# Performance work log

Measured on AMD Instinct MI355X. Metric: run time of the kernel, lower is better.

## Reference

```python
import math
import jax, jax.numpy as jnp
import numpy as np

B, SX, SY, D, H = 2, 1024, 1024, 1024, 16
FULL = 1536   # padded (full_q == full_k) frame length for the two-source attention
N_CTX = 2048  # causal bias buffer size
HD = D // H
LENS_X = np.array([1024, 700])
LENS_Y = np.array([1024, 850])


def _heads(t):
    b, s, d = t.shape
    return t.reshape(b, s, H, HD).transpose(0, 2, 1, 3)  # [B,H,S,HD]


def _merge(t):
    b, h, s, hd = t.shape
    return t.transpose(0, 2, 1, 3).reshape(b, s, h * hd)


def setup_inputs() -> dict:
    key = jax.random.key(0)
    ks = jax.random.split(key, 8)
    s = 0.02
    # ragged pack/unpack index lists: take = positions in the FULL frame, fill = positions in the shrunk frame
    x_take_b = np.concatenate([np.full(l, b, np.int32) for b, l in enumerate(LENS_X)])
    x_take_p = np.concatenate([(FULL - l + np.arange(l)).astype(np.int32) for l in LENS_X])  # right-aligned
    x_fill_b = x_take_b.copy()
    x_fill_p = np.concatenate([np.arange(l, dtype=np.int32) for l in LENS_X])
    y_take_b = np.concatenate([np.full(l, b, np.int32) for b, l in enumerate(LENS_Y)])
    y_take_p = np.concatenate([np.arange(l, dtype=np.int32) for l in LENS_Y])  # left-aligned
    y_fill_b = y_take_b.copy()
    y_fill_p = y_take_p.copy()
    # additive padding mask for the self-attention over shrunk x
    mask = np.full((B, 1, 1, SX), -10000.0, np.float32)
    for b, l in enumerate(LENS_X):
        mask[b, :, :, :l] = 0.0
    return {
        "x": jax.random.normal(ks[0], (B, SX, D), jnp.float32),
        "y": jax.random.normal(ks[1], (B, SY, D), jnp.float32),
        "attention_mask_x": jnp.asarray(mask),
        "W_attn": jax.random.normal(ks[2], (D, 3 * D), jnp.float32) * s,
        "b_attn": jnp.zeros((3 * D,), jnp.float32),
        "W_2a": jax.random.normal(ks[3], (D, D), jnp.float32) * s,
        "b_2a": jnp.zeros((D,), jnp.float32),
        "W_2b": jax.random.normal(ks[4], (D, 2 * D), jnp.float32) * s,
        "b_2b": jnp.zeros((2 * D,), jnp.float32),
        "W_proj": jax.random.normal(ks[5], (2 * D, D), jnp.float32) * s,
        "b_proj": jnp.zeros((D,), jnp.float32),
        "x_take_b": jnp.asarray(x_take_b), "x_take_p": jnp.asarray(x_take_p),
        "x_fill_b": jnp.asarray(x_fill_b), "x_fill_p": jnp.asarray(x_fill_p),
        "y_take_b": jnp.asarray(y_take_b), "y_take_p": jnp.asarray(y_take_p),
        "y_fill_b": jnp.asarray(y_fill_b), "y_fill_p": jnp.asarray(y_fill_p),
    }


def reference(x, y, attention_mask_x, W_attn, b_attn, W_2a, b_2a, W_2b, b_2b,
              W_proj, b_proj, x_take_b, x_take_p, x_fill_b, x_fill_p,
              y_take_b, y_take_p, y_fill_b, y_fill_p):
    causal = jnp.tril(jnp.ones((N_CTX, N_CTX), jnp.float32))
    inv_sqrt = 1.0 / math.sqrt(HD)

    # --- branch 1: causal self-attention on shrunk x ---
    qkv = x @ W_attn + b_attn
    q, k, v = jnp.split(qkv, 3, axis=2)
    q, k, v = _heads(q), _heads(k), _heads(v)
    w = jnp.einsum('bhqd,bhkd->bhqk', q, k) * inv_sqrt  # [B,H,SX,SX]
    b1 = causal[:SX, :SX]
    w = w * b1 - 10000.0 * (1.0 - b1) + attention_mask_x
    a = jnp.einsum('bhqk,bhkd->bhqd', jax.nn.softmax(w, axis=-1), v)
    a = _merge(a)  # [B,SX,D]

    # --- branch 2: two-source attention with ragged expand/shrink ---
    q2 = _heads(x @ W_2a + b_2a)                      # [B,H,SX,HD]
    k2, v2 = jnp.split(y @ W_2b + b_2b, 2, axis=2)
    k2, v2 = _heads(k2), _heads(v2)                   # [B,H,SY,HD]
    w2 = jnp.einsum('bhqd,bhkd->bhqk', q2, k2)        # [B,H,SX,SY] (unscaled yet)
    # expand key dim: shrunk SY -> FULL
    temp = jnp.zeros((B, H, SX, FULL), w2.dtype)
    temp = temp.at[y_take_b, :, :, y_take_p].set(w2[y_fill_b, :, :, y_fill_p])
    # expand query dim: shrunk SX -> FULL
    new_w = jnp.zeros((B, H, FULL, FULL), w2.dtype)
    new_w = new_w.at[x_take_b, :, x_take_p, :].set(temp[x_fill_b, :, x_fill_p, :])
    new_v = jnp.zeros((B, H, FULL, HD), v2.dtype)
    new_v = new_v.at[y_take_b, :, y_take_p, :].set(v2[y_fill_b, :, y_fill_p, :])
    kmask = jnp.full((B, 1, 1, FULL), -10000.0, w2.dtype)
    kmask = kmask.at[y_take_b, :, :, y_take_p].set(0.0)
    new_w = new_w * inv_sqrt
    b2 = causal[:FULL, :FULL]  # ns-nd == 0 since full_q == full_k
    new_w = new_w * b2 - 10000.0 * (1.0 - b2) + kmask
    a2 = jnp.einsum('bhqk,bhkd->bhqd', jax.nn.softmax(new_w, axis=-1), new_v)  # [B,H,FULL,HD]
    # shrink query dim back: FULL -> SX
    a2s = jnp.zeros((B, H, SX, HD), a2.dtype)
    a2s = a2s.at[x_fill_b, :, x_fill_p, :].set(a2[x_take_b, :, x_take_p, :])
    a2m = _merge(a2s)  # [B,SX,D]

    out = jnp.concatenate([a, a2m], axis=2) @ W_proj + b_proj  # [B,SX,D]
    return out
```

## Files before the change

### kernel.cpp

```cpp
#include <hip/hip_runtime.h>
#include <hip/hip_bf16.h>

typedef __bf16 bf16;
typedef __attribute__((ext_vector_type(4))) __bf16 bf16x4;
typedef __attribute__((ext_vector_type(8))) __bf16 bf16x8;
typedef __attribute__((ext_vector_type(4))) float floatx4;

__device__ __forceinline__ void gl_lds16(const bf16* g, bf16* l) {
  __builtin_amdgcn_global_load_lds(
      (const __attribute__((address_space(1))) void*)g,
      (__attribute__((address_space(3))) void*)l, 16, 0, 0);
}

__global__ __launch_bounds__(256) void sentinel_kernel(float* out, int n, float code) {
  int i = blockIdx.x * 256 + threadIdx.x;
  if (i < n) out[i] = code;
}

struct TP { const float* W; bf16* WT; int K; int N; int bxn; int bid0; };

__global__ __launch_bounds__(256) void prep_kernel(TP t0, TP t1, TP t2, TP t3,
                                                   const float* __restrict__ x,
                                                   const float* __restrict__ y,
                                                   bf16* __restrict__ xb,
                                                   bf16* __restrict__ yb) {
  int bid = blockIdx.x;
  int tid = threadIdx.x;
  if (bid < 2048) {
    __shared__ float tile[64][65];
    TP t = t0;
    if (bid >= t3.bid0) t = t3;
    else if (bid >= t2.bid0) t = t2;
    else if (bid >= t1.bid0) t = t1;
    int rb = bid - t.bid0;
    int n0 = (rb % t.bxn) * 64, k0 = (rb / t.bxn) * 64;
    int tx = tid & 15, ty = tid >> 4;
#pragma unroll
    for (int i = 0; i < 4; ++i) {
      floatx4 v = *(const floatx4*)(t.W + (size_t)(k0 + ty + 16 * i) * t.N + n0 + tx * 4);
#pragma unroll
      for (int j = 0; j < 4; ++j) tile[ty + 16 * i][tx * 4 + j] = v[j];
    }
    __syncthreads();
#pragma unroll
    for (int i = 0; i < 4; ++i) {
      int nr = ty + 16 * i;
      bf16x4 o;
#pragma unroll
      for (int j = 0; j < 4; ++j) o[j] = (bf16)tile[tx * 4 + j][nr];
      *(bf16x4*)(t.WT + (size_t)(n0 + nr) * t.K + k0 + tx * 4) = o;
    }
  } else {
    long base = (long)(bid - 2048) * 4096 + (long)tid * 16;
    const float* src = x; bf16* dst = xb; long idx = base;
    if (base >= 2097152) { src = y; dst = yb; idx = base - 2097152; }
    floatx4 v0 = *(const floatx4*)(src + idx);
    floatx4 v1 = *(const floatx4*)(src + idx + 4);
    floatx4 v2 = *(const floatx4*)(src + idx + 8);
    floatx4 v3 = *(const floatx4*)(src + idx + 12);
    bf16x8 o0, o1;
#pragma unroll
    for (int i = 0; i < 4; ++i) {
      o0[i] = (bf16)v0[i]; o0[4 + i] = (bf16)v1[i];
      o1[i] = (bf16)v2[i]; o1[4 + i] = (bf16)v3[i];
    }
    *(bf16x8*)(dst + idx) = o0;
    *(bf16x8*)(dst + idx + 8) = o1;
  }
}

struct GP { const bf16* A; const bf16* WT; const float* bias; bf16* C; bf16* VT;
            int N; int ldc; int vcol0; int bxn; int bid0; };

__global__ __launch_bounds__(256) void proj3_kernel(GP g0, GP g1, GP g2) {
  __shared__ __attribute__((aligned(16))) bf16 As[128 * 64];
  __shared__ __attribute__((aligned(16))) bf16 Bs[128 * 64];
  int bid = blockIdx.x;
  GP g = g0;
  if (bid >= g2.bid0) g = g2;
  else if (bid >= g1.bid0) g = g1;
  int rb = bid - g.bid0;
  int row0 = (rb / g.bxn) * 128, col0 = (rb % g.bxn) * 128;
  const int K = 1024;
  int tid = threadIdx.x;
  int lane = tid & 63, wave = tid >> 6;
  int quad = lane >> 4, l16 = lane & 15;
  int wm = wave >> 1, wn = wave & 1;
  floatx4 acc[4][4] = {};
  for (int k0 = 0; k0 < K; k0 += 64) {
#pragma unroll
    for (int s = 0; s < 4; ++s) {
      int sl = s * 256 + tid;
      int r = sl >> 3, o = sl & 7;
      int c = (o ^ (r & 7)) * 8;
      gl_lds16(g.WT + (size_t)(col0 + r) * K + k0 + c, Bs + (size_t)sl * 8);
      gl_lds16(g.A + (size_t)(row0 + r) * K + k0 + c, As + (size_t)sl * 8);
    }
    __syncthreads();
#pragma unroll
    for (int kk = 0; kk < 2; ++kk) {
      int ko = kk * 4 + quad;
      bf16x8 afr[4], bfr[4];
#pragma unroll
      for (int r = 0; r < 4; ++r) {
        int m = wm * 64 + r * 16 + l16;
        afr[r] = *(const bf16x8*)(As + (size_t)(m * 8 + (ko ^ (m & 7))) * 8);
      }
#pragma unroll
      for (int c = 0; c < 4; ++c) {
        int n = wn * 64 + c * 16 + l16;
        bfr[c] = *(const bf16x8*)(Bs + (size_t)(n * 8 + (ko ^ (n & 7))) * 8);
      }
#pragma unroll
      for (int r = 0; r < 4; ++r)
#pragma unroll
        for (int c = 0; c < 4; ++c)
          acc[r][c] = __builtin_amdgcn_mfma_f32_16x16x32_bf16(afr[r], bfr[c], acc[r][c], 0, 0, 0);
    }
    __syncthreads();
  }
  int inV = (col0 >= g.vcol0);
#pragma unroll
  for (int c = 0; c < 4; ++c) {
    int gcol = col0 + wn * 64 + c * 16 + l16;
    float bv = g.bias[gcol];
    if (inV) {
      int vcol = gcol - g.vcol0;
      int hh = vcol >> 6, dd = vcol & 63;
#pragma unroll
      for (int r = 0; r < 4; ++r) {
        int row = row0 + wm * 64 + r * 16 + quad * 4;
        int bb = row >> 10, key = row & 1023;
        bf16x4 pk;
#pragma unroll
        for (int e = 0; e < 4; ++e) pk[e] = (bf16)(acc[r][c][e] + bv);
        *(bf16x4*)(g.VT + ((size_t)((bb << 4) + hh)) * 65536 + (size_t)dd * 1024 + key) = pk;
      }
    } else {
#pragma unroll
      for (int r = 0; r < 4; ++r) {
        int grow = row0 + wm * 64 + r * 16 + quad * 4;
#pragma unroll
        for (int e = 0; e < 4; ++e)
          g.C[(size_t)(grow + e) * g.ldc + gcol] = (bf16)(acc[r][c][e] + bv);
      }
    }
  }
}

__global__ __launch_bounds__(256) void gemm_out_kernel(const bf16* __restrict__ A,
                                                       const bf16* __restrict__ WT,
                                                       const float* __restrict__ bias,
                                                       float* __restrict__ C,
                                                       int N, int K) {
  __shared__ __attribute__((aligned(16))) bf16 As[64 * 64];
  __shared__ __attribute__((aligned(16))) bf16 Bs[64 * 64];
  int tid = threadIdx.x;
  int lane = tid & 63, wave = tid >> 6;
  int quad = lane >> 4, l16 = lane & 15;
  int row0 = blockIdx.y * 64, col0 = blockIdx.x * 64;
  floatx4 acc[4] = {};
  for (int k0 = 0; k0 < K; k0 += 64) {
#pragma unroll
    for (int s = 0; s < 2; ++s) {
      int sl = s * 256 + tid;
      int r = sl >> 3, o = sl & 7;
      int c = (o ^ (r & 7)) * 8;
      gl_lds16(A + (size_t)(row0 + r) * K + k0 + c, As + (size_t)sl * 8);
      gl_lds16(WT + (size_t)(col0 + r) * K + k0 + c, Bs + (size_t)sl * 8);
    }
    __syncthreads();
#pragma unroll
    for (int kk = 0; kk < 2; ++kk) {
      int ko = kk * 4 + quad;
      int m = wave * 16 + l16;
      bf16x8 af = *(const bf16x8*)(As + (size_t)(m * 8 + (ko ^ (m & 7))) * 8);
#pragma unroll
      for (int nt = 0; nt < 4; ++nt) {
        int n = nt * 16 + l16;
        bf16x8 bf = *(const bf16x8*)(Bs + (size_t)(n * 8 + (ko ^ (n & 7))) * 8);
        acc[nt] = __builtin_amdgcn_mfma_f32_16x16x32_bf16(af, bf, acc[nt], 0, 0, 0);
      }
    }
    __syncthreads();
  }
#pragma unroll
  for (int nt = 0; nt < 4; ++nt) {
    int gcol = col0 + nt * 16 + l16;
    float bv = bias[gcol];
#pragma unroll
    for (int e = 0; e < 4; ++e) {
      int grow = row0 + wave * 16 + quad * 4 + e;
      C[(size_t)grow * N + gcol] = acc[nt][e] + bv;
    }
  }
}

struct AP {
  const bf16* Q; const bf16* K; const bf16* VT; bf16* O;
  int qstride, kstride, ostride;
  long qbatch, kbatch, obatch;
  int coff0, coff1, klen0, klen1, qv0, qv1;
};

__global__ __launch_bounds__(512) void attn2x_kernel(AP a0, AP a1, float scale) {
  __shared__ __attribute__((aligned(16))) bf16 Ks[2][64 * 64];
  __shared__ __attribute__((aligned(16))) bf16 Vs[2][64 * 64];
  __shared__ __attribute__((aligned(16))) bf16 Ps[8][16 * 72];
  AP a = (blockIdx.x >> 8) ? a1 : a0;
  int tid = threadIdx.x;
  int lane = tid & 63, w = tid >> 6;
  int quad = lane >> 4, l16 = lane & 15;
  int r = blockIdx.x & 255;
  int b = r >> 7, h = (r >> 3) & 15, qt = r & 7;
  int coff = b ? a.coff1 : a.coff0;
  int klen = b ? a.klen1 : a.klen0;
  int qv = b ? a.qv1 : a.qv0;
  int qbase = qt * 128;
  int wq0 = qbase + w * 16;
  int qi = wq0 + l16;
  const bf16* Q   = a.Q + (size_t)b * a.qbatch + h * 64;
  const bf16* Kp  = a.K + (size_t)b * a.kbatch + h * 64;
  const bf16* VTp = a.VT + (size_t)(b * 16 + h) * 65536;
  bf16* O = a.O + (size_t)b * a.obatch + h * 64;

  bf16x8 aq0 = *(const bf16x8*)(Q + (size_t)qi * a.qstride + quad * 8);
  bf16x8 aq1 = *(const bf16x8*)(Q + (size_t)qi * a.qstride + 32 + quad * 8);

  floatx4 o[4] = {};
  float part = 0.f;

  int kend = klen < qbase + 128 + coff ? klen : qbase + 128 + coff;
  int nblk = (kend + 63) >> 6;
  int wkend0 = wq0 + 16 + coff;
  int wkend = klen < wkend0 ? klen : wkend0;

  const float KSC = scale * 1.44269504f;
  const float KOFF = -5.77078016f;

  auto stage = [&](int buf, int j0) {
    int row = tid >> 3, ch = tid & 7;
    gl_lds16(Kp + (size_t)(j0 + row) * a.kstride + ((ch ^ (row & 7)) * 8),
             Ks[buf] + (size_t)tid * 8);
    gl_lds16(VTp + (size_t)row * 1024 + j0 + ((ch ^ (row & 7)) * 8),
             Vs[buf] + (size_t)tid * 8);
  };

  stage(0, 0);
  for (int t = 0; t < nblk; ++t) {
    int j0 = t * 64;
    __syncthreads();
    if (t + 1 < nblk) stage((t + 1) & 1, j0 + 64);
    if (j0 >= wkend) continue;
    const bf16* Kt = Ks[t & 1];
    const bf16* Vt = Vs[t & 1];

    floatx4 sv[4];
#pragma unroll
    for (int nt = 0; nt < 4; ++nt) {
      int key = nt * 16 + l16;
      int sl0 = key * 8 + (quad ^ (key & 7));
      int sl1 = key * 8 + ((quad + 4) ^ (key & 7));
      bf16x8 bk0 = *(const bf16x8*)(Kt + (size_t)sl0 * 8);
      bf16x8 bk1 = *(const bf16x8*)(Kt + (size_t)sl1 * 8);
      floatx4 z = {};
      z = __builtin_amdgcn_mfma_f32_16x16x32_bf16(bk0, aq0, z, 0, 0, 0);
      z = __builtin_amdgcn_mfma_f32_16x16x32_bf16(bk1, aq1, z, 0, 0, 0);
      sv[nt] = z;
    }
    bool fullv = (j0 + 63 <= wq0 + coff) && (j0 + 63 < klen);
#pragma unroll
    for (int nt = 0; nt < 4; ++nt) {
      bf16x4 pk;
#pragma unroll
      for (int e = 0; e < 4; ++e) {
        float arg = fmaf(sv[nt][e], KSC, KOFF);
        if (!fullv) {
          int j = j0 + nt * 16 + quad * 4 + e;
          arg = (j <= qi + coff && j < klen) ? arg : -60.0f;
        }
        float p = exp2f(arg);
        part += p;
        pk[e] = (bf16)p;
      }
      *(bf16x4*)(Ps[w] + l16 * 72 + nt * 16 + quad * 4) = pk;
    }
    bf16x8 pb0 = *(const bf16x8*)(Ps[w] + l16 * 72 + quad * 8);
    bf16x8 pb1 = *(const bf16x8*)(Ps[w] + l16 * 72 + 32 + quad * 8);
#pragma unroll
    for (int ct = 0; ct < 4; ++ct) {
      int dd = ct * 16 + l16;
      int sl0 = dd * 8 + (quad ^ (dd & 7));
      int sl1 = dd * 8 + ((quad + 4) ^ (dd & 7));
      bf16x8 va0 = *(const bf16x8*)(Vt + (size_t)sl0 * 8);
      bf16x8 va1 = *(const bf16x8*)(Vt + (size_t)sl1 * 8);
      o[ct] = __builtin_amdgcn_mfma_f32_16x16x32_bf16(va0, pb0, o[ct], 0, 0, 0);
      o[ct] = __builtin_amdgcn_mfma_f32_16x16x32_bf16(va1, pb1, o[ct], 0, 0, 0);
    }
  }
  part += __shfl_xor(part, 16);
  part += __shfl_xor(part, 32);
  float rinv = 1.0f / part;
#pragma unroll
  for (int ct = 0; ct < 4; ++ct) {
    bf16x4 pk;
#pragma unroll
    for (int e = 0; e < 4; ++e) {
      float val = o[ct][e] * rinv;
      if (qi >= qv) val = 0.f;
      pk[e] = (bf16)val;
    }
    *(bf16x4*)(O + (size_t)qi * a.ostride + ct * 16 + quad * 4) = pk;
  }
}

extern "C" void kernel_launch(void* const* d_in, const int* in_sizes, int n_in,
                              void* d_out, int out_size, void* d_ws, size_t ws_size,
                              hipStream_t stream) {
  const float* x      = (const float*)d_in[0];
  const float* y      = (const float*)d_in[1];
  const float* W_attn = (const float*)d_in[3];
  const float* b_attn = (const float*)d_in[4];
  const float* W_2a   = (const float*)d_in[5];
  const float* b_2a   = (const float*)d_in[6];
  const float* W_2b   = (const float*)d_in[7];
  const float* b_2b   = (const float*)d_in[8];
  const float* W_proj = (const float*)d_in[9];
  const float* b_proj = (const float*)d_in[10];
  bf16* ws = (bf16*)d_ws;
  float* out = (float*)d_out;

  const int LX0 = 1024, LX1 = 700, LY0 = 1024, LY1 = 850;
  const float scale = 0.125f;
  const size_t WS_FAST = (size_t)25165824 * 2;

  if (ws_size < WS_FAST) {
    sentinel_kernel<<<(out_size + 255) / 256, 256, 0, stream>>>(
        out, out_size, (float)(ws_size >> 20) + 10.0f);
    return;
  }

  bf16* qk1  = ws;
  bf16* q2   = ws + (size_t) 4194304;
  bf16* k2   = ws + (size_t) 6291456;
  bf16* VT1  = ws + (size_t) 8388608;
  bf16* VT2  = ws + (size_t)10485760;
  bf16* xb   = ws + (size_t)12582912;
  bf16* yb   = ws + (size_t)14680064;
  bf16* cat  = ws + (size_t)12582912;
  bf16* WaT  = ws + (size_t)16777216;
  bf16* W2aT = ws + (size_t)19922944;
  bf16* W2bT = ws + (size_t)20971520;
  bf16* WpT  = ws + (size_t)23068672;

  TP t0 = {W_attn, WaT, 1024, 3072, 48, 0};
  TP t1 = {W_2a, W2aT, 1024, 1024, 16, 768};
  TP t2 = {W_2b, W2bT, 1024, 2048, 32, 1024};
  TP t3 = {W_proj, WpT, 2048, 1024, 16, 1536};
  prep_kernel<<<3072, 256, 0, stream>>>(t0, t1, t2, t3, x, y, xb, yb);

  GP g0 = {xb, WaT, b_attn, qk1, VT1, 3072, 2048, 2048, 24, 0};
  GP g1 = {xb, W2aT, b_2a, q2, nullptr, 1024, 1024, 1 << 30, 8, 384};
  GP g2 = {yb, W2bT, b_2b, k2, VT2, 2048, 1024, 1024, 16, 512};
  proj3_kernel<<<768, 256, 0, stream>>>(g0, g1, g2);

  AP a0 = {qk1, qk1 + 1024, VT1, cat, 2048, 2048, 2048,
           (long)1024 * 2048, (long)1024 * 2048, (long)1024 * 2048,
           0, 0, LX0, LX1, 1024, 1024};
  AP a1 = {q2, k2, VT2, cat + 1024, 1024, 1024, 2048,
           (long)1024 * 1024, (long)1024 * 1024, (long)1024 * 2048,
           1536 - LX0, 1536 - LX1, LY0, LY1, LX0, LX1};
  attn2x_kernel<<<512, 512, 0, stream>>>(a0, a1, scale);

  gemm_out_kernel<<<dim3(16, 32), 256, 0, stream>>>(cat, WpT, b_proj, out, 1024, 2048);
}
```

Before: 233.8 us.

## Retile output GEMM, swizzle block order, stage stores through LDS, add MFMA priority

The output projection GEMM moves from 64x64 to 128x64 tiles with a 2x2 wave layout, launched as 256 blocks in an XCD-interleaved order. The fused projection kernel also gets an interleaved block order and occupancy hint 3. Its non-V outputs are staged through LDS so each lane writes 16-byte rows instead of scattered 2-byte stores. The attention kernel reverses the query-tile order for the second source to balance causal work, and raises wave priority around MFMA sections. Together these target L2 locality, store coalescing and load balance, at the cost of fewer blocks in the final GEMM and more register pressure.

```diff
diff --git a/kernel.cpp b/kernel.cpp
--- a/kernel.cpp
+++ b/kernel.cpp
@@ -72,29 +72,33 @@
 struct GP { const bf16* A; const bf16* WT; const float* bias; bf16* C; bf16* VT;
             int N; int ldc; int vcol0; int bxn; int bid0; };
 
-__global__ __launch_bounds__(256) void proj3_kernel(GP g0, GP g1, GP g2) {
+__global__ __launch_bounds__(256, 3) void proj3_kernel(GP g0, GP g1, GP g2) {
   __shared__ __attribute__((aligned(16))) bf16 As[128 * 64];
   __shared__ __attribute__((aligned(16))) bf16 Bs[128 * 64];
-  int bid = blockIdx.x;
+  int rawb = blockIdx.x;
+  int bid = (rawb & 7) * 96 + (rawb >> 3);
   GP g = g0;
   if (bid >= g2.bid0) g = g2;
   else if (bid >= g1.bid0) g = g1;
   int rb = bid - g.bid0;
   int row0 = (rb / g.bxn) * 128, col0 = (rb % g.bxn) * 128;
-  const int K = 1024;
   int tid = threadIdx.x;
   int lane = tid & 63, wave = tid >> 6;
   int quad = lane >> 4, l16 = lane & 15;
   int wm = wave >> 1, wn = wave & 1;
+  const bf16* Ag = g.A + (size_t)row0 * 1024;
+  const bf16* Bg = g.WT + (size_t)col0 * 1024;
+
   floatx4 acc[4][4] = {};
-  for (int k0 = 0; k0 < K; k0 += 64) {
+
+  for (int k0 = 0; k0 < 1024; k0 += 64) {
 #pragma unroll
     for (int s = 0; s < 4; ++s) {
       int sl = s * 256 + tid;
       int r = sl >> 3, o = sl & 7;
       int c = (o ^ (r & 7)) * 8;
-      gl_lds16(g.WT + (size_t)(col0 + r) * K + k0 + c, Bs + (size_t)sl * 8);
-      gl_lds16(g.A + (size_t)(row0 + r) * K + k0 + c, As + (size_t)sl * 8);
+      gl_lds16(Ag + (size_t)r * 1024 + k0 + c, As + (size_t)sl * 8);
+      gl_lds16(Bg + (size_t)r * 1024 + k0 + c, Bs + (size_t)sl * 8);
     }
     __syncthreads();
 #pragma unroll
@@ -119,12 +123,13 @@
     }
     __syncthreads();
   }
+
   int inV = (col0 >= g.vcol0);
-#pragma unroll
-  for (int c = 0; c < 4; ++c) {
-    int gcol = col0 + wn * 64 + c * 16 + l16;
-    float bv = g.bias[gcol];
-    if (inV) {
+  if (inV) {
+#pragma unroll
+    for (int c = 0; c < 4; ++c) {
+      int gcol = col0 + wn * 64 + c * 16 + l16;
+      float bv = g.bias[gcol];
       int vcol = gcol - g.vcol0;
       int hh = vcol >> 6, dd = vcol & 63;
 #pragma unroll
@@ -136,14 +141,29 @@
         for (int e = 0; e < 4; ++e) pk[e] = (bf16)(acc[r][c][e] + bv);
         *(bf16x4*)(g.VT + ((size_t)((bb << 4) + hh)) * 65536 + (size_t)dd * 1024 + key) = pk;
       }
-    } else {
-#pragma unroll
-      for (int r = 0; r < 4; ++r) {
-        int grow = row0 + wm * 64 + r * 16 + quad * 4;
+    }
+  } else {
+    bf16* S = ((bf16*)As) + wave * 1152;
+    float bvv[4];
+#pragma unroll
+    for (int c = 0; c < 4; ++c) bvv[c] = g.bias[col0 + wn * 64 + c * 16 + l16];
+#pragma unroll
+    for (int r = 0; r < 4; ++r) {
+#pragma unroll
+      for (int c = 0; c < 4; ++c)
 #pragma unroll
         for (int e = 0; e < 4; ++e)
-          g.C[(size_t)(grow + e) * g.ldc + gcol] = (bf16)(acc[r][c][e] + bv);
-      }
+          S[(quad * 4 + e) * 72 + c * 16 + l16] = (bf16)(acc[r][c][e] + bvv[c]);
+      asm volatile("s_waitcnt lgkmcnt(0)" ::: "memory");
+      int R0 = row0 + wm * 64 + r * 16;
+#pragma unroll
+      for (int t = 0; t < 2; ++t) {
+        int s = t * 64 + lane;
+        int rr = s >> 3, q = s & 7;
+        bf16x8 vv = *(const bf16x8*)(S + rr * 72 + q * 8);
+        *(bf16x8*)(g.C + (size_t)(R0 + rr) * g.ldc + col0 + wn * 64 + q * 8) = vv;
+      }
+      asm volatile("s_waitcnt lgkmcnt(0)" ::: "memory");
     }
   }
 }
@@ -151,47 +171,62 @@
 __global__ __launch_bounds__(256) void gemm_out_kernel(const bf16* __restrict__ A,
                                                        const bf16* __restrict__ WT,
                                                        const float* __restrict__ bias,
-                                                       float* __restrict__ C,
-                                                       int N, int K) {
-  __shared__ __attribute__((aligned(16))) bf16 As[64 * 64];
+                                                       float* __restrict__ C) {
+  const int K = 2048;
+  __shared__ __attribute__((aligned(16))) bf16 As[128 * 64];
   __shared__ __attribute__((aligned(16))) bf16 Bs[64 * 64];
+  int raw = blockIdx.x;
+  int bid = (raw & 7) * 32 + (raw >> 3);
+  int row0 = (bid >> 4) * 128;
+  int col0 = (bid & 15) * 64;
   int tid = threadIdx.x;
   int lane = tid & 63, wave = tid >> 6;
   int quad = lane >> 4, l16 = lane & 15;
-  int row0 = blockIdx.y * 64, col0 = blockIdx.x * 64;
-  floatx4 acc[4] = {};
+  int wm = wave >> 1, wn = wave & 1;
+  floatx4 acc[4][2] = {};
   for (int k0 = 0; k0 < K; k0 += 64) {
 #pragma unroll
-    for (int s = 0; s < 2; ++s) {
+    for (int s = 0; s < 4; ++s) {
       int sl = s * 256 + tid;
       int r = sl >> 3, o = sl & 7;
       int c = (o ^ (r & 7)) * 8;
       gl_lds16(A + (size_t)(row0 + r) * K + k0 + c, As + (size_t)sl * 8);
-      gl_lds16(WT + (size_t)(col0 + r) * K + k0 + c, Bs + (size_t)sl * 8);
+      if (s < 2)
+        gl_lds16(WT + (size_t)(col0 + r) * K + k0 + c, Bs + (size_t)sl * 8);
     }
     __syncthreads();
 #pragma unroll
     for (int kk = 0; kk < 2; ++kk) {
       int ko = kk * 4 + quad;
-      int m = wave * 16 + l16;
-      bf16x8 af = *(const bf16x8*)(As + (size_t)(m * 8 + (ko ^ (m & 7))) * 8);
-#pragma unroll
-      for (int nt = 0; nt < 4; ++nt) {
-        int n = nt * 16 + l16;
-        bf16x8 bf = *(const bf16x8*)(Bs + (size_t)(n * 8 + (ko ^ (n & 7))) * 8);
-        acc[nt] = __builtin_amdgcn_mfma_f32_16x16x32_bf16(af, bf, acc[nt], 0, 0, 0);
-      }
-    }
-    __syncthreads();
-  }
-#pragma unroll
-  for (int nt = 0; nt < 4; ++nt) {
-    int gcol = col0 + nt * 16 + l16;
+      bf16x8 afr[4], bfr[2];
+#pragma unroll
+      for (int r = 0; r < 4; ++r) {
+        int m = wm * 64 + r * 16 + l16;
+        afr[r] = *(const bf16x8*)(As + (size_t)(m * 8 + (ko ^ (m & 7))) * 8);
+      }
+#pragma unroll
+      for (int c = 0; c < 2; ++c) {
+        int n = wn * 32 + c * 16 + l16;
+        bfr[c] = *(const bf16x8*)(Bs + (size_t)(n * 8 + (ko ^ (n & 7))) * 8);
+      }
+#pragma unroll
+      for (int r = 0; r < 4; ++r)
+#pragma unroll
+        for (int c = 0; c < 2; ++c)
+          acc[r][c] = __builtin_amdgcn_mfma_f32_16x16x32_bf16(afr[r], bfr[c], acc[r][c], 0, 0, 0);
+    }
+    __syncthreads();
+  }
+#pragma unroll
+  for (int c = 0; c < 2; ++c) {
+    int gcol = col0 + wn * 32 + c * 16 + l16;
     float bv = bias[gcol];
 #pragma unroll
-    for (int e = 0; e < 4; ++e) {
-      int grow = row0 + wave * 16 + quad * 4 + e;
-      C[(size_t)grow * N + gcol] = acc[nt][e] + bv;
+    for (int r = 0; r < 4; ++r) {
+      int grow = row0 + wm * 64 + r * 16 + quad * 4;
+#pragma unroll
+      for (int e = 0; e < 4; ++e)
+        C[(size_t)(grow + e) * 1024 + gcol] = acc[r][c][e] + bv;
     }
   }
 }
@@ -207,12 +242,14 @@
   __shared__ __attribute__((aligned(16))) bf16 Ks[2][64 * 64];
   __shared__ __attribute__((aligned(16))) bf16 Vs[2][64 * 64];
   __shared__ __attribute__((aligned(16))) bf16 Ps[8][16 * 72];
-  AP a = (blockIdx.x >> 8) ? a1 : a0;
+  int grp = blockIdx.x >> 8;
+  AP a = grp ? a1 : a0;
   int tid = threadIdx.x;
   int lane = tid & 63, w = tid >> 6;
   int quad = lane >> 4, l16 = lane & 15;
   int r = blockIdx.x & 255;
   int b = r >> 7, h = (r >> 3) & 15, qt = r & 7;
+  if (grp) qt = 7 - qt;
   int coff = b ? a.coff1 : a.coff0;
   int klen = b ? a.klen1 : a.klen0;
   int qv = b ? a.qv1 : a.qv0;
@@ -256,6 +293,7 @@
     const bf16* Vt = Vs[t & 1];
 
     floatx4 sv[4];
+    __builtin_amdgcn_s_setprio(1);
 #pragma unroll
     for (int nt = 0; nt < 4; ++nt) {
       int key = nt * 16 + l16;
@@ -268,6 +306,7 @@
       z = __builtin_amdgcn_mfma_f32_16x16x32_bf16(bk1, aq1, z, 0, 0, 0);
       sv[nt] = z;
     }
+    __builtin_amdgcn_s_setprio(0);
     bool fullv = (j0 + 63 <= wq0 + coff) && (j0 + 63 < klen);
 #pragma unroll
     for (int nt = 0; nt < 4; ++nt) {
@@ -287,6 +326,7 @@
     }
     bf16x8 pb0 = *(const bf16x8*)(Ps[w] + l16 * 72 + quad * 8);
     bf16x8 pb1 = *(const bf16x8*)(Ps[w] + l16 * 72 + 32 + quad * 8);
+    __builtin_amdgcn_s_setprio(1);
 #pragma unroll
     for (int ct = 0; ct < 4; ++ct) {
       int dd = ct * 16 + l16;
@@ -297,6 +337,7 @@
       o[ct] = __builtin_amdgcn_mfma_f32_16x16x32_bf16(va0, pb0, o[ct], 0, 0, 0);
       o[ct] = __builtin_amdgcn_mfma_f32_16x16x32_bf16(va1, pb1, o[ct], 0, 0, 0);
     }
+    __builtin_amdgcn_s_setprio(0);
   }
   part += __shfl_xor(part, 16);
   part += __shfl_xor(part, 32);
@@ -372,5 +413,5 @@
            1536 - LX0, 1536 - LX1, LY0, LY1, LX0, LX1};
   attn2x_kernel<<<512, 512, 0, stream>>>(a0, a1, scale);
 
-  gemm_out_kernel<<<dim3(16, 32), 256, 0, stream>>>(cat, WpT, b_proj, out, 1024, 2048);
-}
+  gemm_out_kernel<<<256, 256, 0, stream>>>(cat, WpT, b_proj, out);
+}
```

After: 216.7 us. 1.08x faster.
